# Kernel tuning notes

Measured on AMD Instinct MI355X. Metric: run time of the kernel, lower is better.

## Reference

```python
import jax, jax.numpy as jnp
import numpy as np

B, T, TEMP_IN, STAT_IN = 8, 512, 32, 16
TEMP_H, STAT_H, ATTN_H, N_LAYERS, N_CLS = 64, 32, 32, 2, 2
BN_INV = float(1.0 / np.sqrt(1.0 + 1e-5))  # eval-mode BN, running_mean=0, running_var=1


def _bn(x, g, b):
    return x * (g * BN_INV) + b


def _lrelu(x):
    return jax.nn.leaky_relu(x, 0.01)


def _mlp_layer(x, W, b, g, beta):
    return _lrelu(_bn(x @ W + b, g, beta))


def setup_inputs() -> dict:
    key = jax.random.key(0)
    ks = jax.random.split(key, 32)
    lengths = jax.random.randint(ks[0], (B,), T // 2, T + 1)
    mask_q = jnp.arange(T)[None, :] < lengths[:, None]          # [B,T]
    masks = mask_q[:, :, None]                                   # [B,T,1] bool
    x_temp = jax.random.normal(ks[1], (B, T, TEMP_IN), jnp.float32) * mask_q[..., None]
    x_stat = jax.random.normal(ks[2], (B, STAT_IN), jnp.float32)
    t = jnp.sort(jax.random.uniform(ks[3], (B, T), jnp.float32) * 100.0, axis=-1)
    p = lambda k, sh, s=0.1: jax.random.normal(k, sh, jnp.float32) * s
    inp = dict(x_temp=x_temp, x_stat=x_stat, t=t, masks=masks, lengths=lengths)
    # attn_mlp: Linear(1,H)+BN+LeakyReLU, Linear(H,1)
    inp['aw0'] = p(ks[4], (1, ATTN_H), 0.5); inp['ab0'] = p(ks[5], (ATTN_H,))
    inp['ag'] = 1.0 + p(ks[6], (ATTN_H,)); inp['abeta'] = p(ks[7], (ATTN_H,))
    inp['aw1'] = p(ks[8], (ATTN_H, 1), 0.2); inp['ab1'] = p(ks[9], (1,))
    # top non_linear_temp / non_linear_stat
    inp['tw'] = p(ks[10], (TEMP_IN, TEMP_H)); inp['tb'] = p(ks[11], (TEMP_H,))
    inp['tg'] = 1.0 + p(ks[12], (TEMP_H,)); inp['tbeta'] = p(ks[13], (TEMP_H,))
    inp['sw'] = p(ks[14], (STAT_IN, STAT_H)); inp['sb'] = p(ks[15], (STAT_H,))
    inp['sg'] = 1.0 + p(ks[16], (STAT_H,)); inp['sbeta'] = p(ks[17], (STAT_H,))
    # stacked SimtaPlusLayer params [L,...]
    inp['lw_t'] = p(ks[18], (N_LAYERS, TEMP_H + STAT_H, TEMP_H))
    inp['lb_t'] = p(ks[19], (N_LAYERS, TEMP_H))
    inp['lg_t'] = 1.0 + p(ks[20], (N_LAYERS, TEMP_H)); inp['lbeta_t'] = p(ks[21], (N_LAYERS, TEMP_H))
    inp['lw_s'] = p(ks[22], (N_LAYERS, STAT_H, STAT_H))
    inp['lb_s'] = p(ks[23], (N_LAYERS, STAT_H))
    inp['lg_s'] = 1.0 + p(ks[24], (N_LAYERS, STAT_H)); inp['lbeta_s'] = p(ks[25], (N_LAYERS, STAT_H))
    inp['cw'] = p(ks[26], (TEMP_H + STAT_H, N_CLS)); inp['cb'] = p(ks[27], (N_CLS,))
    return inp


def _forward(x_temp, x_stat, t, aw0, ab0, ag, abeta, aw1, ab1, tw, tb, tg, tbeta,
             sw, sb, sg, sbeta, lw_t, lb_t, lg_t, lbeta_t, lw_s, lb_s, lg_s, lbeta_s,
             cw, cb, mask_q):
    # dt[b,i,j] = (t[b,j]-t[b,i]) / (max dt + eps)
    dt = t[:, None, :] - t[:, :, None]
    dt = dt / (dt.max() + 1e-8)
    # pairwise-MLP temporal attention: [B,T,T,H] intermediate (memory-bound)
    h = _lrelu(_bn(dt[..., None] * aw0[0] + ab0, ag, abeta))
    a = (h @ aw1)[..., 0] + ab1[0]                                # [B,T,T]
    temp_attn = jax.nn.softmax(jnp.where(mask_q[:, None, :], a, -9e8), axis=-1)

    x_t = _mlp_layer(x_temp, tw, tb, tg, tbeta)                   # [B,T,Ct]
    x_s = _mlp_layer(x_stat, sw, sb, sg, sbeta)                   # [B,Cs]

    for l in range(lw_t.shape[0]):
        xs_rep = jnp.broadcast_to(x_s[:, None, :], (x_t.shape[0], x_t.shape[1], x_s.shape[-1]))
        x = _mlp_layer(jnp.concatenate([x_t, xs_rep], axis=-1), lw_t[l], lb_t[l], lg_t[l], lbeta_t[l])
        x = x * mask_q[..., None]                                 # pad_packed zeros invalid rows
        d = jnp.asarray(x.shape[-1], x.dtype)
        qk = jnp.einsum('bic,bjc->bij', x, x) / jnp.sqrt(d)
        self_attn = jax.nn.softmax(qk, axis=-1)                   # torch softmaxes over all keys (pads give qk=0)
        attn = (self_attn + temp_attn) * mask_q[:, None, :]       # masked_fill(~mask, 0) on key columns
        x_s = _mlp_layer(x_s, lw_s[l], lb_s[l], lg_s[l], lbeta_s[l])
        x_t = (attn @ x) * mask_q[..., None]

    xs_rep = jnp.broadcast_to(x_s[:, None, :], (x_t.shape[0], x_t.shape[1], x_s.shape[-1]))
    output = jnp.concatenate([x_t, xs_rep], axis=-1) @ cw + cb    # [B,T,C]
    output = output * mask_q[..., None]
    # per-segment argmax over (logit1 - logit0), gather that row
    diff = jnp.where(mask_q, output[..., 1] - output[..., 0], -1e30)
    idx = jnp.argmax(diff, axis=1)                                # [B]
    output_max = output[jnp.arange(output.shape[0]), idx]         # [B,C]
    return output, output_max


def reference(x_temp, x_stat, t, masks, lengths, aw0, ab0, ag, abeta, aw1, ab1,
              tw, tb, tg, tbeta, sw, sb, sg, sbeta,
              lw_t, lb_t, lg_t, lbeta_t, lw_s, lb_s, lg_s, lbeta_s, cw, cb):
    mask_q = jnp.any(masks, axis=-1)                              # [B,T]
    return _forward(x_temp, x_stat, t, aw0, ab0, ag, abeta, aw1, ab1, tw, tb, tg, tbeta,
                    sw, sb, sg, sbeta, lw_t, lb_t, lg_t, lbeta_t, lw_s, lb_s, lg_s, lbeta_s,
                    cw, cb, mask_q)
```

## Files before the change

### kernel.cpp

```cpp
#include <hip/hip_runtime.h>

#define B 8
#define T 512
#define TEMP_IN 32
#define STAT_IN 16
#define TEMP_H 64
#define STAT_H 32
#define ATTN_H 32
#define N_CLS 2
#define BN_INV 0.99999500003749969f
#define R 4
#define NTILE (T / R)

struct KP {
    const float *x_temp, *x_stat, *t;
    const int* lengths;
    const float *aw0, *ab0, *ag, *abeta, *aw1, *ab1;
    const float *tw, *tb, *tg, *tbeta;
    const float *sw, *sb, *sg, *sbeta;
    const float *lw_t, *lb_t, *lg_t, *lbeta_t;
    const float *lw_s, *lb_s, *lg_s, *lbeta_s;
    const float *cw, *cb;
    float *XL, *XL2;
    unsigned long long* cand;
    unsigned *f1, *f2;
    unsigned *arr;
    float *out, *outmax;
};

__device__ __forceinline__ float lrelu(float x) {
    return fmaxf(x, 0.01f * x);
}
__device__ __forceinline__ float wave_max(float x) {
    #pragma unroll
    for (int o = 32; o > 0; o >>= 1) x = fmaxf(x, __shfl_xor(x, o));
    return x;
}
__device__ __forceinline__ float wave_sum(float x) {
    #pragma unroll
    for (int o = 32; o > 0; o >>= 1) x += __shfl_xor(x, o);
    return x;
}
__device__ __forceinline__ unsigned ordf(float f) {
    unsigned u = __float_as_uint(f);
    return (u & 0x80000000u) ? ~u : (u | 0x80000000u);
}
__device__ __forceinline__ void stg_llc(float* p, float v) {
    __hip_atomic_store(p, v, __ATOMIC_RELAXED, __HIP_MEMORY_SCOPE_AGENT);
}
__device__ __forceinline__ float ldg_llc(const float* p) {
    return __hip_atomic_load(p, __ATOMIC_RELAXED, __HIP_MEMORY_SCOPE_AGENT);
}
__device__ __forceinline__ void drain_vm() {
    asm volatile("s_waitcnt vmcnt(0)" ::: "memory");
}
__device__ __forceinline__ void fence_acq_wg() {
    __builtin_amdgcn_fence(__ATOMIC_ACQUIRE, "workgroup");
}

struct Shm {
    float att[R][T];
    float part[4][R][TEMP_H];
    float xi[R][TEMP_H];
    float x1[R][TEMP_H];
    float t_s[T];
    float s_w[3 * ATTN_H + 1];
    float xs[3][STAT_H];
    float xr[4][TEMP_IN];
    float h0s[4][TEMP_H + STAT_H];
    float o_rc[R][2];
    int lastf;
};

__device__ __forceinline__ void publish(unsigned* f) {
    drain_vm();
    __syncthreads();
    if (threadIdx.x == 0)
        __hip_atomic_store(f, 1u, __ATOMIC_RELAXED, __HIP_MEMORY_SCOPE_AGENT);
}
__device__ __forceinline__ void wait_batch(const unsigned* fbase, int tid) {
    if (tid < NTILE) {
        const unsigned* p = fbase + tid * 16;
        while (__hip_atomic_load(p, __ATOMIC_RELAXED, __HIP_MEMORY_SCOPE_AGENT) == 0u)
            __builtin_amdgcn_s_sleep(4);
    }
    __syncthreads();
    fence_acq_wg();
}

__device__ __forceinline__ void front(const KP& P, Shm& S, int b, int i0, int len,
                                      int lane, int wave) {
    int i = i0 + wave;
    int row = b * T + i;
    if (lane < TEMP_IN) S.xr[wave][lane] = P.x_temp[row * TEMP_IN + lane];
    __syncthreads();
    float acc = P.tb[lane];
    #pragma unroll
    for (int k = 0; k < TEMP_IN; ++k) acc += S.xr[wave][k] * P.tw[k * TEMP_H + lane];
    acc = acc * (P.tg[lane] * BN_INV) + P.tbeta[lane];
    S.h0s[wave][lane] = lrelu(acc);
    if (lane < STAT_H) S.h0s[wave][TEMP_H + lane] = S.xs[0][lane];
    __syncthreads();
    float a2 = P.lb_t[lane];
    #pragma unroll
    for (int k = 0; k < TEMP_H + STAT_H; ++k) a2 += S.h0s[wave][k] * P.lw_t[k * TEMP_H + lane];
    a2 = a2 * (P.lg_t[lane] * BN_INV) + P.lbeta_t[lane];
    a2 = lrelu(a2);
    stg_llc(&P.XL[(size_t)row * TEMP_H + lane], (i < len) ? a2 : 0.f);
    __syncthreads();
}

__device__ __forceinline__ void temp_compute(Shm& S, float tmpv[8], float inv_dt,
                                             int i0, int len, int lane, int wave) {
    float ab1v = S.s_w[3 * ATTN_H];
    float ti = S.t_s[i0 + wave];
    float a[8], dtq[8];
    #pragma unroll
    for (int q = 0; q < 8; ++q) {
        dtq[q] = (S.t_s[lane + q * 64] - ti) * inv_dt;
        a[q] = ab1v;
    }
    #pragma unroll 4
    for (int k = 0; k < ATTN_H; ++k) {
        float Wk = S.s_w[k];
        float Ck = S.s_w[ATTN_H + k];
        float w1k = S.s_w[2 * ATTN_H + k];
        #pragma unroll
        for (int q = 0; q < 8; ++q) {
            float h = dtq[q] * Wk + Ck;
            h = fmaxf(h, 0.01f * h);
            a[q] += h * w1k;
        }
    }
    float m2 = -1e30f;
    #pragma unroll
    for (int q = 0; q < 8; ++q) {
        int j = lane + q * 64;
        a[q] = (j < len) ? a[q] : -9e8f;
        m2 = fmaxf(m2, a[q]);
    }
    m2 = wave_max(m2);
    float s2 = 0.f;
    #pragma unroll
    for (int q = 0; q < 8; ++q) { a[q] = __expf(a[q] - m2); s2 += a[q]; }
    s2 = wave_sum(s2);
    float inv2 = 1.0f / s2;
    #pragma unroll
    for (int q = 0; q < 8; ++q) tmpv[q] = a[q] * inv2;
}

template <int EPI, bool LOAD_XI>
__device__ __forceinline__ void attn_core(const KP& P, Shm& S, const float* src,
                                          const float tmpv[8],
                                          int b, int i0, int len, int tid, int lane, int wave,
                                          int blk_id) {
    if (LOAD_XI) {
        if (tid < R * TEMP_H)
            S.xi[tid >> 6][tid & 63] = src[((size_t)(b * T + i0 + (tid >> 6))) * TEMP_H + (tid & 63)];
    }
    __syncthreads();
    for (int j = tid; j < T; j += 256) {
        const float4* xj4 = reinterpret_cast<const float4*>(&src[((size_t)(b * T + j)) * TEMP_H]);
        float acc[R];
        #pragma unroll
        for (int r = 0; r < R; ++r) acc[r] = 0.f;
        #pragma unroll
        for (int c4 = 0; c4 < TEMP_H / 4; ++c4) {
            float4 xv = xj4[c4];
            #pragma unroll
            for (int r = 0; r < R; ++r) {
                float4 xi4 = *reinterpret_cast<const float4*>(&S.xi[r][c4 * 4]);
                acc[r] += xi4.x * xv.x + xi4.y * xv.y + xi4.z * xv.z + xi4.w * xv.w;
            }
        }
        #pragma unroll
        for (int r = 0; r < R; ++r) S.att[r][j] = acc[r] * 0.125f;
    }
    __syncthreads();
    {
        int r = wave;
        float v[8];
        float m = -1e30f;
        #pragma unroll
        for (int q = 0; q < 8; ++q) { v[q] = S.att[r][lane + q * 64]; m = fmaxf(m, v[q]); }
        m = wave_max(m);
        float s = 0.f;
        #pragma unroll
        for (int q = 0; q < 8; ++q) { v[q] = __expf(v[q] - m); s += v[q]; }
        s = wave_sum(s);
        float invs = 1.0f / s;
        #pragma unroll
        for (int q = 0; q < 8; ++q) {
            int j = lane + q * 64;
            S.att[r][j] = (j < len) ? (v[q] * invs + tmpv[q]) : 0.f;
        }
    }
    __syncthreads();
    float acc2[R];
    #pragma unroll
    for (int r = 0; r < R; ++r) acc2[r] = 0.f;
    {
        const float* srow = src + (size_t)b * T * TEMP_H + lane;
        int j0 = wave * 128;
        for (int g = 0; g < 32; ++g) {
            int j = j0 + g * 4;
            float xv0 = srow[(size_t)(j + 0) * TEMP_H];
            float xv1 = srow[(size_t)(j + 1) * TEMP_H];
            float xv2 = srow[(size_t)(j + 2) * TEMP_H];
            float xv3 = srow[(size_t)(j + 3) * TEMP_H];
            #pragma unroll
            for (int r = 0; r < R; ++r) {
                float4 a4 = *reinterpret_cast<const float4*>(&S.att[r][j]);
                acc2[r] += a4.x * xv0 + a4.y * xv1 + a4.z * xv2 + a4.w * xv3;
            }
        }
    }
    #pragma unroll
    for (int r = 0; r < R; ++r) S.part[wave][r][lane] = acc2[r];
    __syncthreads();
    {
        int r = wave, cc = lane;
        float sum = S.part[0][r][cc] + S.part[1][r][cc] + S.part[2][r][cc] + S.part[3][r][cc];
        S.x1[r][cc] = ((i0 + r) < len) ? sum : 0.f;
    }
    __syncthreads();

    if (EPI == 0) {
        const float* lw1    = P.lw_t + (TEMP_H + STAT_H) * TEMP_H;
        const float* lb1    = P.lb_t + TEMP_H;
        const float* lg1    = P.lg_t + TEMP_H;
        const float* lbeta1 = P.lbeta_t + TEMP_H;
        int r = wave;
        int i = i0 + r;
        float acc = lb1[lane];
        #pragma unroll
        for (int k = 0; k < TEMP_H; ++k) acc += S.x1[r][k] * lw1[k * TEMP_H + lane];
        #pragma unroll
        for (int k = 0; k < STAT_H; ++k) acc += S.xs[1][k] * lw1[(TEMP_H + k) * TEMP_H + lane];
        acc = acc * (lg1[lane] * BN_INV) + lbeta1[lane];
        acc = lrelu(acc);
        float vout = (i < len) ? acc : 0.f;
        stg_llc(&P.XL2[((size_t)(b * T + i)) * TEMP_H + lane], vout);
        __syncthreads();
        S.xi[r][lane] = vout;
    } else {
        if (tid < R * N_CLS) {
            int r = tid >> 1, cls = tid & 1;
            int i = i0 + r;
            float o = P.cb[cls];
            #pragma unroll
            for (int k = 0; k < TEMP_H; ++k) o += S.x1[r][k] * P.cw[k * N_CLS + cls];
            #pragma unroll
            for (int k = 0; k < STAT_H; ++k) o += S.xs[2][k] * P.cw[(TEMP_H + k) * N_CLS + cls];
            if (i >= len) o = 0.f;
            stg_llc(&P.out[((size_t)(b * T + i)) * N_CLS + cls], o);
            S.o_rc[r][cls] = o;
        }
        __syncthreads();
        if (tid == 0) {
            float best = -3e30f; int bi = i0;
            for (int r = 0; r < R; ++r) {
                int i = i0 + r;
                float diff = (i < len) ? (S.o_rc[r][1] - S.o_rc[r][0]) : -1e30f;
                if (diff > best) { best = diff; bi = i; }
            }
            unsigned long long pack =
                ((unsigned long long)ordf(best) << 32) | (unsigned)(~(unsigned)bi);
            __hip_atomic_store(&P.cand[blk_id * 8], pack,
                               __ATOMIC_RELAXED, __HIP_MEMORY_SCOPE_AGENT);
            drain_vm();
            unsigned old = __hip_atomic_fetch_add(&P.arr[b * 16], 1u,
                                                  __ATOMIC_RELAXED, __HIP_MEMORY_SCOPE_AGENT);
            S.lastf = (old == (NTILE - 1)) ? 1 : 0;
        }
        __syncthreads();
        if (S.lastf) {
            fence_acq_wg();
            if (tid < 64) {
                unsigned long long c0 = __hip_atomic_load(&P.cand[(b * NTILE + tid) * 8],
                                                          __ATOMIC_RELAXED, __HIP_MEMORY_SCOPE_AGENT);
                unsigned long long c1 = __hip_atomic_load(&P.cand[(b * NTILE + 64 + tid) * 8],
                                                          __ATOMIC_RELAXED, __HIP_MEMORY_SCOPE_AGENT);
                unsigned long long c = (c1 > c0) ? c1 : c0;
                #pragma unroll
                for (int o = 32; o > 0; o >>= 1) {
                    unsigned long long oc = __shfl_xor(c, o);
                    c = (oc > c) ? oc : c;
                }
                if (tid == 0) {
                    int idx = (int)(~(unsigned)(c & 0xffffffffu));
                    float o0 = ldg_llc(&P.out[((size_t)(b * T + idx)) * N_CLS + 0]);
                    float o1 = ldg_llc(&P.out[((size_t)(b * T + idx)) * N_CLS + 1]);
                    stg_llc(&P.outmax[b * 2 + 0], o0);
                    stg_llc(&P.outmax[b * 2 + 1], o1);
                }
            }
        }
    }
}

template <int PHASE>
__global__ void __launch_bounds__(256, 4) k_run(KP P) {
    __shared__ Shm S;
    int tid = threadIdx.x, lane = tid & 63, wave = tid >> 6;
    int blk = blockIdx.x;
    int b = blk & 7, tile = blk >> 3, i0 = tile * R;
    int blk_id = b * NTILE + tile;
    int len = P.lengths[b];
    float tmpv[8];

    if (tid < STAT_H) {
        float acc = P.sb[tid];
        #pragma unroll
        for (int k = 0; k < STAT_IN; ++k) acc += P.x_stat[b * STAT_IN + k] * P.sw[k * STAT_H + tid];
        acc = acc * (P.sg[tid] * BN_INV) + P.sbeta[tid];
        S.xs[0][tid] = lrelu(acc);
    }
    __syncthreads();

    if (PHASE == 0 || PHASE == 3) front(P, S, b, i0, len, lane, wave);
    if (PHASE == 3) publish(&P.f1[blk_id * 16]);

    if (PHASE != 0) {
        if (tid < ATTN_H) {
            float g = P.ag[tid] * BN_INV;
            S.s_w[tid]              = P.aw0[tid] * g;
            S.s_w[ATTN_H + tid]     = P.ab0[tid] * g + P.abeta[tid];
            S.s_w[2 * ATTN_H + tid] = P.aw1[tid];
        }
        if (tid == 0) S.s_w[3 * ATTN_H] = P.ab1[0];
        S.t_s[tid] = P.t[b * T + tid];
        S.t_s[tid + 256] = P.t[b * T + tid + 256];
        float d = P.t[(lane & 7) * T + (T - 1)] - P.t[(lane & 7) * T];
        d = wave_max(d);
        float inv_dt = 1.0f / (d + 1e-8f);
        __syncthreads();
        if (tid < STAT_H) {
            float a2 = P.lb_s[tid];
            #pragma unroll
            for (int k = 0; k < STAT_H; ++k) a2 += S.xs[0][k] * P.lw_s[k * STAT_H + tid];
            a2 = a2 * (P.lg_s[tid] * BN_INV) + P.lbeta_s[tid];
            S.xs[1][tid] = lrelu(a2);
        }
        __syncthreads();
        if (tid < STAT_H) {
            float a2 = P.lb_s[STAT_H + tid];
            #pragma unroll
            for (int k = 0; k < STAT_H; ++k) a2 += S.xs[1][k] * P.lw_s[(STAT_H + k) * STAT_H + tid];
            a2 = a2 * (P.lg_s[STAT_H + tid] * BN_INV) + P.lbeta_s[STAT_H + tid];
            S.xs[2][tid] = lrelu(a2);
        }
        __syncthreads();
        temp_compute(S, tmpv, inv_dt, i0, len, lane, wave);
        __syncthreads();
    }

    if (PHASE == 3) wait_batch(P.f1 + b * NTILE * 16, tid);
    if (PHASE == 1 || PHASE == 3)
        attn_core<0, true>(P, S, P.XL, tmpv, b, i0, len, tid, lane, wave, blk_id);
    if (PHASE == 3) {
        publish(&P.f2[blk_id * 16]);
        wait_batch(P.f2 + b * NTILE * 16, tid);
        attn_core<1, false>(P, S, P.XL2, tmpv, b, i0, len, tid, lane, wave, blk_id);
    } else if (PHASE == 2) {
        attn_core<1, true>(P, S, P.XL2, tmpv, b, i0, len, tid, lane, wave, blk_id);
    }
}

extern "C" void kernel_launch(void* const* d_in, const int* in_sizes, int n_in,
                              void* d_out, int out_size, void* d_ws, size_t ws_size,
                              hipStream_t stream) {
    KP p;
    p.x_temp  = (const float*)d_in[0];
    p.x_stat  = (const float*)d_in[1];
    p.t       = (const float*)d_in[2];
    p.lengths = (const int*)d_in[4];
    p.aw0 = (const float*)d_in[5];
    p.ab0 = (const float*)d_in[6];
    p.ag  = (const float*)d_in[7];
    p.abeta = (const float*)d_in[8];
    p.aw1 = (const float*)d_in[9];
    p.ab1 = (const float*)d_in[10];
    p.tw  = (const float*)d_in[11];
    p.tb  = (const float*)d_in[12];
    p.tg  = (const float*)d_in[13];
    p.tbeta = (const float*)d_in[14];
    p.sw  = (const float*)d_in[15];
    p.sb  = (const float*)d_in[16];
    p.sg  = (const float*)d_in[17];
    p.sbeta = (const float*)d_in[18];
    p.lw_t = (const float*)d_in[19];
    p.lb_t = (const float*)d_in[20];
    p.lg_t = (const float*)d_in[21];
    p.lbeta_t = (const float*)d_in[22];
    p.lw_s = (const float*)d_in[23];
    p.lb_s = (const float*)d_in[24];
    p.lg_s = (const float*)d_in[25];
    p.lbeta_s = (const float*)d_in[26];
    p.cw = (const float*)d_in[27];
    p.cb = (const float*)d_in[28];

    float* ws = (float*)d_ws;
    p.XL  = ws;
    p.XL2 = ws + (size_t)B * T * TEMP_H;
    p.cand = (unsigned long long*)(ws + 2 * (size_t)B * T * TEMP_H);
    p.f1  = (unsigned*)(p.cand + B * NTILE * 8);
    p.f2  = p.f1 + B * NTILE * 16;
    p.arr = p.f2 + B * NTILE * 16;
    p.out = (float*)d_out;
    p.outmax = p.out + (size_t)B * T * N_CLS;

    size_t flagbytes = (size_t)B * NTILE * 8 * 8
                     + 2 * (size_t)B * NTILE * 16 * 4 + (size_t)B * 16 * 4;
    hipMemsetAsync(p.cand, 0, flagbytes, stream);

    void* args[] = { (void*)&p };
    hipError_t err = hipLaunchCooperativeKernel((const void*)k_run<3>, dim3(B * NTILE),
                                                dim3(256), args, 0, stream);
    if (err != hipSuccess) {
        (void)hipGetLastError();
        k_run<0><<<B * NTILE, 256, 0, stream>>>(p);
        k_run<1><<<B * NTILE, 256, 0, stream>>>(p);
        k_run<2><<<B * NTILE, 256, 0, stream>>>(p);
    }
}
```

Baseline: 101.1 us.

## Transpose attention tile in LDS and vectorize attn@x over float4 columns

Stores the attention scores in LDS as [T][R] so the four query rows for each key sit together and can be read and written as one float4. The attn@x product is re-partitioned so each thread handles four output columns over a 32-key chunk with float4 global loads, instead of one scalar column over 128 keys. The 16 per-chunk partial results are then reduced through a larger LDS partial buffer. This trades scalar strided loads and repeated LDS reads for vector loads, at the cost of more LDS and a longer final reduction.

```diff
diff --git a/kernel.cpp b/kernel.cpp
--- a/kernel.cpp
+++ b/kernel.cpp
@@ -59,8 +59,8 @@
 }
 
 struct Shm {
-    float att[R][T];
-    float part[4][R][TEMP_H];
+    float att_t[T][R];
+    float part[16][R][TEMP_H];
     float xi[R][TEMP_H];
     float x1[R][TEMP_H];
     float t_s[T];
@@ -173,8 +173,8 @@
                 acc[r] += xi4.x * xv.x + xi4.y * xv.y + xi4.z * xv.z + xi4.w * xv.w;
             }
         }
-        #pragma unroll
-        for (int r = 0; r < R; ++r) S.att[r][j] = acc[r] * 0.125f;
+        float4 av = { acc[0] * 0.125f, acc[1] * 0.125f, acc[2] * 0.125f, acc[3] * 0.125f };
+        *reinterpret_cast<float4*>(&S.att_t[j][0]) = av;
     }
     __syncthreads();
     {
@@ -182,7 +182,7 @@
         float v[8];
         float m = -1e30f;
         #pragma unroll
-        for (int q = 0; q < 8; ++q) { v[q] = S.att[r][lane + q * 64]; m = fmaxf(m, v[q]); }
+        for (int q = 0; q < 8; ++q) { v[q] = S.att_t[lane + q * 64][r]; m = fmaxf(m, v[q]); }
         m = wave_max(m);
         float s = 0.f;
         #pragma unroll
@@ -192,35 +192,35 @@
         #pragma unroll
         for (int q = 0; q < 8; ++q) {
             int j = lane + q * 64;
-            S.att[r][j] = (j < len) ? (v[q] * invs + tmpv[q]) : 0.f;
-        }
-    }
-    __syncthreads();
-    float acc2[R];
-    #pragma unroll
-    for (int r = 0; r < R; ++r) acc2[r] = 0.f;
+            S.att_t[j][r] = (j < len) ? (v[q] * invs + tmpv[q]) : 0.f;
+        }
+    }
+    __syncthreads();
     {
-        const float* srow = src + (size_t)b * T * TEMP_H + lane;
-        int j0 = wave * 128;
-        for (int g = 0; g < 32; ++g) {
-            int j = j0 + g * 4;
-            float xv0 = srow[(size_t)(j + 0) * TEMP_H];
-            float xv1 = srow[(size_t)(j + 1) * TEMP_H];
-            float xv2 = srow[(size_t)(j + 2) * TEMP_H];
-            float xv3 = srow[(size_t)(j + 3) * TEMP_H];
-            #pragma unroll
-            for (int r = 0; r < R; ++r) {
-                float4 a4 = *reinterpret_cast<const float4*>(&S.att[r][j]);
-                acc2[r] += a4.x * xv0 + a4.y * xv1 + a4.z * xv2 + a4.w * xv3;
-            }
-        }
-    }
-    #pragma unroll
-    for (int r = 0; r < R; ++r) S.part[wave][r][lane] = acc2[r];
+        int c4 = tid & 15, jc = tid >> 4;
+        float4 acc4[R];
+        #pragma unroll
+        for (int r = 0; r < R; ++r) acc4[r] = float4{0.f, 0.f, 0.f, 0.f};
+        const float* sbase = src + (size_t)b * T * TEMP_H + c4 * 4;
+        int j0 = jc * 32;
+        for (int j = j0; j < j0 + 32; ++j) {
+            float4 xv = *reinterpret_cast<const float4*>(&sbase[(size_t)j * TEMP_H]);
+            float4 av = *reinterpret_cast<const float4*>(&S.att_t[j][0]);
+            acc4[0].x += av.x * xv.x; acc4[0].y += av.x * xv.y; acc4[0].z += av.x * xv.z; acc4[0].w += av.x * xv.w;
+            acc4[1].x += av.y * xv.x; acc4[1].y += av.y * xv.y; acc4[1].z += av.y * xv.z; acc4[1].w += av.y * xv.w;
+            acc4[2].x += av.z * xv.x; acc4[2].y += av.z * xv.y; acc4[2].z += av.z * xv.z; acc4[2].w += av.z * xv.w;
+            acc4[3].x += av.w * xv.x; acc4[3].y += av.w * xv.y; acc4[3].z += av.w * xv.z; acc4[3].w += av.w * xv.w;
+        }
+        #pragma unroll
+        for (int r = 0; r < R; ++r)
+            *reinterpret_cast<float4*>(&S.part[jc][r][c4 * 4]) = acc4[r];
+    }
     __syncthreads();
     {
         int r = wave, cc = lane;
-        float sum = S.part[0][r][cc] + S.part[1][r][cc] + S.part[2][r][cc] + S.part[3][r][cc];
+        float sum = 0.f;
+        #pragma unroll
+        for (int jc = 0; jc < 16; ++jc) sum += S.part[jc][r][cc];
         S.x1[r][cc] = ((i0 + r) < len) ? sum : 0.f;
     }
     __syncthreads();
```

New measurement: 112.0 us. 1.11x slower.
